# Optimization experiments

Measured on AMD Instinct MI355X. Metric: run time of the kernel, lower is better.

## Reference

```python
import jax, jax.numpy as jnp
import numpy as np

P = 8          # patch_size
DIM = 256      # embed dim
HEADS = 8
HEAD_DIM = DIM // HEADS
CH = 3
PATCH_DIM = CH * P * P  # 192
INNER = int(4.0 * DIM)  # 1024
SCALE = HEAD_DIM ** -0.5


def sine_pos_embedding(n, c, dtype=jnp.float32):
    # standard 1D sinusoidal position encoding, shape (n, c)
    pos = jnp.arange(n, dtype=jnp.float32)[:, None]            # (n,1)
    div = jnp.exp(jnp.arange(0, c, 2, dtype=jnp.float32) * (-np.log(10000.0) / c))
    pe = jnp.zeros((n, c), dtype=jnp.float32)
    pe = pe.at[:, 0::2].set(jnp.sin(pos * div))
    pe = pe.at[:, 1::2].set(jnp.cos(pos * div))
    return pe.astype(dtype)


def patchify(x):
    # (B,C,H,W) -> (B, n, p1*p2*C), matching 'b c (h p1) (w p2) -> b (h w) (p1 p2 c)'
    B, C, H, W = x.shape
    hp, wp = H // P, W // P
    x = x.reshape(B, C, hp, P, wp, P)
    x = x.transpose(0, 2, 4, 3, 5, 1)        # (B, hp, wp, p1, p2, C)
    return x.reshape(B, hp * wp, P * P * C)


def unpatchify(x, hp, wp):
    # (B, n, p1*p2*C) -> (B, C, H, W)
    B = x.shape[0]
    x = x.reshape(B, hp, wp, P, P, CH)
    x = x.transpose(0, 5, 1, 3, 2, 4)        # (B, C, hp, p1, wp, p2)
    return x.reshape(B, CH, hp * P, wp * P)


def setup_inputs() -> dict:
    key = jax.random.key(0)
    ks = jax.random.split(key, 16)
    B, H, W = 8, 256, 256
    s = 0.02
    img0 = jax.random.normal(ks[0], (B, CH, H, W), dtype=jnp.float32)
    img1 = jax.random.normal(ks[1], (B, CH, H, W), dtype=jnp.float32)
    mask = jax.random.randint(ks[2], (B, 1, H, W), 0, 2).astype(jnp.float32)
    return {
        "img0": img0,
        "img1": img1,
        "mask": mask,
        "w_patch": jax.random.normal(ks[3], (PATCH_DIM, DIM), jnp.float32) * s,
        "b_patch": jnp.zeros((DIM,), jnp.float32),
        "w_kv": jax.random.normal(ks[4], (DIM, 2 * DIM), jnp.float32) * s,
        "b_kv": jnp.zeros((2 * DIM,), jnp.float32),
        "w_qv": jax.random.normal(ks[5], (DIM, 2 * DIM), jnp.float32) * s,
        "b_qv": jnp.zeros((2 * DIM,), jnp.float32),
        "w_fc1": jax.random.normal(ks[6], (DIM, INNER), jnp.float32) * s,
        "b_fc1": jnp.zeros((INNER,), jnp.float32),
        "w_fc2": jax.random.normal(ks[7], (INNER, PATCH_DIM), jnp.float32) * s,
        "b_fc2": jnp.zeros((PATCH_DIM,), jnp.float32),
    }


def reference(img0, img1, mask, w_patch, b_patch, w_kv, b_kv, w_qv, b_qv,
              w_fc1, b_fc1, w_fc2, b_fc2):
    B, C, H, W = img0.shape
    hp, wp = H // P, W // P
    n = hp * wp

    x0 = patchify(img0) @ w_patch + b_patch   # (B, n, dim)
    x1 = patchify(img1) @ w_patch + b_patch
    pe = sine_pos_embedding(n, DIM)
    x0 = x0 + pe
    x1 = x1 + pe

    # img0 -> k, v
    kv = (x0 @ w_kv + b_kv).reshape(B, n, 2, HEADS, HEAD_DIM)
    kv = kv.transpose(2, 0, 3, 1, 4)          # (2, B, heads, n, hd)
    k, v = kv[0], kv[1]

    # img1 -> q (v1 unused in forward, matching torch code)
    qv = (x1 @ w_qv + b_qv).reshape(B, n, 2, DIM).transpose(2, 0, 1, 3)
    q = qv[0].reshape(B, n, HEADS, HEAD_DIM).transpose(0, 2, 1, 3)  # (B, heads, n, hd)

    dots = jnp.einsum('bhqd,bhkd->bhqk', q, k) * SCALE  # (B, heads, n, n)

    # mask: (B,1,H,W) -> per-patch sum -> binary -> additive bias over key dim
    msum = mask.reshape(B, 1, hp, P, wp, P).sum(axis=(3, 5)).reshape(B, 1, n)
    bias = jnp.where(msum > 0, 0.0, -100.0)[:, :, None, :]  # (B,1,1,n)

    attn = jax.nn.softmax(dots + bias, axis=-1)
    out = jnp.einsum('bhqk,bhkd->bhqd', attn, v)
    out = out.transpose(0, 2, 1, 3).reshape(B, n, DIM)

    # mlp2: Linear -> GELU(exact) -> Linear
    h = jax.nn.gelu(out @ w_fc1 + b_fc1, approximate=False)
    res = h @ w_fc2 + b_fc2                   # (B, n, patch_dim)

    return unpatchify(res, hp, wp)            # (B, C, H, W)
```

## Files before the change

### kernel.cpp

```cpp
#include <hip/hip_runtime.h>
#include <cstdint>
#include <cstddef>

typedef __bf16 bf16_t;
typedef uint32_t u32;
typedef __bf16 bf16x4 __attribute__((ext_vector_type(4)));
typedef __bf16 bf16x8 __attribute__((ext_vector_type(8)));
typedef float f32x4 __attribute__((ext_vector_type(4)));
typedef float f32x16 __attribute__((ext_vector_type(16)));

__device__ __forceinline__ void gload_lds16(const bf16_t* g, bf16_t* l) {
  __builtin_amdgcn_global_load_lds((const __attribute__((address_space(1))) void*)g,
                                   (__attribute__((address_space(3))) void*)l,
                                   16, 0, 0);
}

__device__ __forceinline__ f32x4 mfma16(bf16x8 a, bf16x8 b, f32x4 c) {
  return __builtin_amdgcn_mfma_f32_16x16x32_bf16(a, b, c, 0, 0, 0);
}
__device__ __forceinline__ f32x16 mfma32(bf16x8 a, bf16x8 b, f32x16 c) {
  return __builtin_amdgcn_mfma_f32_32x32x16_bf16(a, b, c, 0, 0, 0);
}

#define LOG2E 1.4426950408889634f

__global__ __launch_bounds__(256)
void prep_all(const float* __restrict__ img0, const float* __restrict__ img1,
              const float* __restrict__ mask,
              const float* __restrict__ wp, const float* __restrict__ wkv,
              const float* __restrict__ wqv, const float* __restrict__ wfc1,
              const float* __restrict__ wfc2,
              bf16_t* __restrict__ xp0, bf16_t* __restrict__ xp1,
              float* __restrict__ pe, float* __restrict__ bias,
              bf16_t* __restrict__ wpT, bf16_t* __restrict__ wkvT,
              bf16_t* __restrict__ wqT, bf16_t* __restrict__ wfc1T,
              bf16_t* __restrict__ wfc2T) {
  __shared__ float tl[64 * 65];
  int bid = blockIdx.x, tid = threadIdx.x;
  if (bid < 1536) {
    int imgsel = bid >= 768;
    int t = (bid - (imgsel ? 768 : 0)) * 256 + tid;
    const float* img = imgsel ? img1 : img0;
    bf16_t* xp = imgsel ? xp1 : xp0;
    int wpp = t & 31, p1 = (t >> 5) & 7, hp = (t >> 8) & 31, rest = t >> 13;
    int b = rest / 3, c = rest - b * 3;
    const float* src = img + (((size_t)(b * 3 + c) * 256 + hp * 8 + p1) * 256 + wpp * 8);
    float4 v0 = *(const float4*)src;
    float4 v1 = *(const float4*)(src + 4);
    int row = b * 1024 + hp * 32 + wpp;
    bf16_t* dst = xp + (size_t)row * 192 + p1 * 24 + c;
    dst[0]  = (bf16_t)v0.x; dst[3]  = (bf16_t)v0.y; dst[6]  = (bf16_t)v0.z; dst[9]  = (bf16_t)v0.w;
    dst[12] = (bf16_t)v1.x; dst[15] = (bf16_t)v1.y; dst[18] = (bf16_t)v1.z; dst[21] = (bf16_t)v1.w;
  } else if (bid < 2560) {
    int t = bid - 1536, c = tid;
    int i2 = c & ~1;
    float div = expf((float)i2 * (-9.210340371976184f / 256.0f));
    float arg = (float)t * div;
    pe[t * 256 + c] = (c & 1) ? cosf(arg) : sinf(arg);
  } else if (bid < 2592) {
    int g = (bid - 2560) * 256 + tid;
    int b = g >> 10, t = g & 1023, hp = t >> 5, wpp = t & 31;
    const float* mp = mask + ((size_t)b * 256 + hp * 8) * 256 + wpp * 8;
    float s = 0.f;
    #pragma unroll
    for (int p1 = 0; p1 < 8; p1++) {
      float4 a = *(const float4*)(mp + p1 * 256);
      float4 c = *(const float4*)(mp + p1 * 256 + 4);
      s += a.x + a.y + a.z + a.w + c.x + c.y + c.z + c.w;
    }
    bias[g] = (s > 0.f) ? 0.f : (-100.f * LOG2E);
  } else {
    int i = bid - 2592;
    const float* src; bf16_t* dst; int srcN, dstK, NT;
    if (i >= 172) {
      int j = i - 172;
      bf16_t* p = wfc2T + 192 * 1024 + j * 8192 + tid * 32;
      bf16x8 z;
      #pragma unroll
      for (int e = 0; e < 8; e++) z[e] = (bf16_t)0.0f;
      *(bf16x8*)(p) = z; *(bf16x8*)(p + 8) = z;
      *(bf16x8*)(p + 16) = z; *(bf16x8*)(p + 24) = z;
      return;
    }
    if (i < 12)       { src = wp;   dst = wpT;   srcN = 256;  dstK = 192;  NT = 4; }
    else if (i < 44)  { i -= 12;  src = wkv;  dst = wkvT;  srcN = 512;  dstK = 256;  NT = 8; }
    else if (i < 60)  { i -= 44;  src = wqv;  dst = wqT;   srcN = 512;  dstK = 256;  NT = 4; }
    else if (i < 124) { i -= 60;  src = wfc1; dst = wfc1T; srcN = 1024; dstK = 256;  NT = 16; }
    else              { i -= 124; src = wfc2; dst = wfc2T; srcN = 192;  dstK = 1024; NT = 3; }
    int kt = i / NT, nt = i - kt * NT;
    #pragma unroll
    for (int j = 0; j < 4; j++) {
      int r = (tid >> 4) + 16 * j, c = (tid & 15) * 4;
      float4 v = *(const float4*)(src + (size_t)(kt * 64 + r) * srcN + nt * 64 + c);
      tl[r * 65 + c] = v.x; tl[r * 65 + c + 1] = v.y;
      tl[r * 65 + c + 2] = v.z; tl[r * 65 + c + 3] = v.w;
    }
    __syncthreads();
    #pragma unroll
    for (int j = 0; j < 16; j++) {
      int flat = tid + 256 * j;
      int n_l = flat >> 6, k_l = flat & 63;
      dst[(size_t)(nt * 64 + n_l) * dstK + kt * 64 + k_l] = (bf16_t)tl[k_l * 65 + n_l];
    }
  }
}

template<int EPI, int BN>
__global__ __launch_bounds__(256)
void gemm_bt(const bf16_t* __restrict__ A_, const bf16_t* __restrict__ A2,
             const bf16_t* __restrict__ Bt_, const bf16_t* __restrict__ Bt2,
             int M, int N, int K,
             const float* __restrict__ bias_, const float* __restrict__ bias2,
             const float* __restrict__ pe,
             bf16_t* __restrict__ out_b, bf16_t* __restrict__ out_b2,
             bf16_t* __restrict__ out_b3, float* __restrict__ out_f) {
  constexpr int NF = BN / 32;
  __shared__ bf16_t alds[4 * 64 * 8];
  __shared__ bf16_t blds[4 * BN * 8];
  const int tid = threadIdx.x;
  const int lane = tid & 63, wid = tid >> 6;
  const int ln15 = lane & 15, hi = lane >> 4;
  const int brow = blockIdx.x * 64;
  int bcol = blockIdx.y * BN;
  const bf16_t* A = A_;
  const bf16_t* Bt = Bt_;
  const float* bias = bias_;
  bool qpart = false;
  if (EPI == 0 && blockIdx.z) A = A2;
  if (EPI == 5 && blockIdx.y >= 4) {
    qpart = true; A = A2; Bt = Bt2; bias = bias2; bcol -= 512;
  }
  const int wr = wid >> 1, wc = wid & 1;

  f32x4 acc[2][NF];
  #pragma unroll
  for (int m = 0; m < 2; m++)
    #pragma unroll
    for (int n = 0; n < NF; n++) acc[m][n] = (f32x4){0.f, 0.f, 0.f, 0.f};

  for (int k0 = 0; k0 < K; k0 += 32) {
    {
      int c = tid; int row = c & 63; int kb = c >> 6;
      const bf16_t* g = A + (size_t)(brow + row) * K + k0 + kb * 8;
      gload_lds16(g, &alds[(wid * 64) * 8]);
    }
    #pragma unroll
    for (int s = 0; s < BN / 64; s++) {
      int c = tid + s * 256; int row = c & (BN - 1); int kb = c / BN;
      const bf16_t* g = Bt + (size_t)(bcol + row) * K + k0 + kb * 8;
      gload_lds16(g, &blds[(wid * 64 + s * 256) * 8]);
    }
    __syncthreads();
    bf16x8 af[2], bfr[NF];
    #pragma unroll
    for (int m = 0; m < 2; m++)
      af[m] = *(const bf16x8*)&alds[(hi * 64 + wr * 32 + m * 16 + ln15) * 8];
    #pragma unroll
    for (int n = 0; n < NF; n++)
      bfr[n] = *(const bf16x8*)&blds[(hi * BN + wc * (BN / 2) + n * 16 + ln15) * 8];
    #pragma unroll
    for (int m = 0; m < 2; m++)
      #pragma unroll
      for (int n = 0; n < NF; n++)
        acc[m][n] = mfma16(af[m], bfr[n], acc[m][n]);
    __syncthreads();
  }

  #pragma unroll
  for (int m = 0; m < 2; m++) {
    #pragma unroll
    for (int n = 0; n < NF; n++) {
      #pragma unroll
      for (int r = 0; r < 4; r++) {
        int grow = brow + wr * 32 + m * 16 + hi * 4 + r;
        int gcol = bcol + wc * (BN / 2) + n * 16 + ln15;
        float v = acc[m][n][r];
        if (EPI == 0) {
          v += bias[gcol] + pe[(grow & 1023) * 256 + gcol];
          bf16_t* outx = blockIdx.z ? out_b2 : out_b;
          outx[(size_t)grow * N + gcol] = (bf16_t)v;
        } else if (EPI == 5) {
          v += bias[gcol];
          int b = grow >> 10, t = grow & 1023;
          if (!qpart) {
            if (gcol < 256) {
              int h = gcol >> 5, d = gcol & 31;
              out_b[(((size_t)(b * 8 + h) * 1024 + t) << 5) + d] = (bf16_t)v;
            } else {
              int c2 = gcol - 256; int h = c2 >> 5, d = c2 & 31;
              out_b2[(((size_t)(b * 8 + h) * 32 + d) << 10) + t] = (bf16_t)v;
            }
          } else {
            v *= (0.17677669529663687f * LOG2E);
            int h = gcol >> 5, d = gcol & 31;
            out_b3[(((size_t)(b * 8 + h) * 1024 + t) << 5) + d] = (bf16_t)v;
          }
        } else if (EPI == 3) {
          v += bias[gcol];
          float gg = 0.5f * v * (1.0f + erff(v * 0.7071067811865476f));
          out_b[(size_t)grow * N + gcol] = (bf16_t)gg;
        } else if (EPI == 4) {
          if (gcol < 192) {
            v += bias[gcol];
            int b = grow >> 10, t = grow & 1023;
            int hp = t >> 5, wpp = t & 31;
            int p = gcol / 3; int c = gcol - p * 3;
            int p1 = p >> 3, p2 = p & 7;
            out_f[(((size_t)(b * 3 + c) * 256 + hp * 8 + p1) * 256) + wpp * 8 + p2] = v;
          }
        }
      }
    }
  }
}

struct Ld { bf16x8 kA, kB, vA, vB; f32x4 c0, c1, c2, c3; };

__device__ __forceinline__ void ldstep(int k0, const bf16_t* kb, const bf16_t* vb,
                                       const float* bb, int l31, int g, Ld& L) {
  L.kA = *(const bf16x8*)(kb + (size_t)(k0 + l31) * 32 + g * 8);
  L.kB = *(const bf16x8*)(kb + (size_t)(k0 + l31) * 32 + 16 + g * 8);
  L.vA = *(const bf16x8*)(vb + (size_t)l31 * 1024 + k0 + g * 8);
  L.vB = *(const bf16x8*)(vb + (size_t)l31 * 1024 + k0 + 16 + g * 8);
  L.c0 = *(const f32x4*)(bb + k0 + 4 * g);
  L.c1 = *(const f32x4*)(bb + k0 + 8 + 4 * g);
  L.c2 = *(const f32x4*)(bb + k0 + 16 + 4 * g);
  L.c3 = *(const f32x4*)(bb + k0 + 24 + 4 * g);
}

union PW { u32 w[4]; bf16x8 v; };

__device__ __forceinline__ u32 pkbf(float a, float b) {
  union { bf16_t h[2]; u32 w; } u;
  u.h[0] = (bf16_t)a; u.h[1] = (bf16_t)b;
  return u.w;
}

__device__ __forceinline__ void step(const Ld& L, bf16x8 qf0, bf16x8 qf1, int g,
                                     f32x16& acc, f32x16& lacc, bf16x8 onesb) {
  f32x16 S;
  S[0] = L.c0[0]; S[1] = L.c0[1]; S[2] = L.c0[2]; S[3] = L.c0[3];
  S[4] = L.c1[0]; S[5] = L.c1[1]; S[6] = L.c1[2]; S[7] = L.c1[3];
  S[8] = L.c2[0]; S[9] = L.c2[1]; S[10] = L.c2[2]; S[11] = L.c2[3];
  S[12] = L.c3[0]; S[13] = L.c3[1]; S[14] = L.c3[2]; S[15] = L.c3[3];
  S = mfma32(L.kA, qf0, S);
  S = mfma32(L.kB, qf1, S);
  float p[16];
  #pragma unroll
  for (int r = 0; r < 16; r++) p[r] = exp2f(S[r]);
  u32 w[8];
  #pragma unroll
  for (int j = 0; j < 8; j++) w[j] = pkbf(p[2 * j], p[2 * j + 1]);
  u32 t0 = (u32)__shfl_xor((int)(g ? w[0] : w[2]), 32);
  u32 t1 = (u32)__shfl_xor((int)(g ? w[1] : w[3]), 32);
  u32 t2 = (u32)__shfl_xor((int)(g ? w[4] : w[6]), 32);
  u32 t3 = (u32)__shfl_xor((int)(g ? w[5] : w[7]), 32);
  PW A0, A1;
  A0.w[0] = g ? t0 : w[0];  A0.w[1] = g ? t1 : w[1];
  A0.w[2] = g ? w[2] : t0;  A0.w[3] = g ? w[3] : t1;
  A1.w[0] = g ? t2 : w[4];  A1.w[1] = g ? t3 : w[5];
  A1.w[2] = g ? w[6] : t2;  A1.w[3] = g ? w[7] : t3;
  acc = mfma32(A0.v, L.vA, acc);
  acc = mfma32(A1.v, L.vB, acc);
  lacc = mfma32(A0.v, onesb, lacc);
  lacc = mfma32(A1.v, onesb, lacc);
}

__global__ __launch_bounds__(256)
void attn_kernel(const bf16_t* __restrict__ q, const bf16_t* __restrict__ k,
                 const bf16_t* __restrict__ vt, const float* __restrict__ bias,
                 bf16_t* __restrict__ out) {
  int tid = threadIdx.x, lane = tid & 63, wid = tid >> 6;
  int l31 = lane & 31, g = lane >> 5;
  int x = blockIdx.x & 7, idx = blockIdx.x >> 3;
  int qb = idx & 7;
  int bh = ((idx >> 3) << 3) | x;
  int b = bh >> 3, h = bh & 7;
  int q0 = qb * 128 + wid * 32;
  const bf16_t* qp = q + ((size_t)bh * 1024 + q0 + l31) * 32;
  bf16x8 qf0 = *(const bf16x8*)(qp + g * 8);
  bf16x8 qf1 = *(const bf16x8*)(qp + 16 + g * 8);
  const bf16_t* kbase = k + (size_t)bh * 32768;
  const bf16_t* vbase = vt + (size_t)bh * 32768;
  const float* bb = bias + b * 1024;

  bf16x8 onesb;
  #pragma unroll
  for (int e = 0; e < 8; e++) onesb[e] = (bf16_t)1.0f;
  f32x16 acc, lacc;
  #pragma unroll
  for (int r = 0; r < 16; r++) { acc[r] = 0.f; lacc[r] = 0.f; }

  Ld La, Lb;
  ldstep(0, kbase, vbase, bb, l31, g, La);
  for (int kt = 0; kt < 32; kt += 2) {
    ldstep((kt + 1) * 32, kbase, vbase, bb, l31, g, Lb);
    step(La, qf0, qf1, g, acc, lacc, onesb);
    int nx = (kt + 2 < 32) ? (kt + 2) * 32 : 31 * 32;
    ldstep(nx, kbase, vbase, bb, l31, g, La);
    step(Lb, qf0, qf1, g, acc, lacc, onesb);
  }

  #pragma unroll
  for (int r = 0; r < 16; r++) {
    int row = (r & 3) + 8 * (r >> 2) + 4 * g;
    float o = acc[r] / lacc[r];
    out[((size_t)b * 1024 + q0 + row) * 256 + h * 32 + l31] = (bf16_t)o;
  }
}

extern "C" void kernel_launch(void* const* d_in, const int* in_sizes, int n_in,
                              void* d_out, int out_size, void* d_ws, size_t ws_size,
                              hipStream_t stream) {
  (void)in_sizes; (void)n_in; (void)out_size; (void)ws_size;
  const float* img0    = (const float*)d_in[0];
  const float* img1    = (const float*)d_in[1];
  const float* mask    = (const float*)d_in[2];
  const float* w_patch = (const float*)d_in[3];
  const float* b_patch = (const float*)d_in[4];
  const float* w_kv    = (const float*)d_in[5];
  const float* b_kv    = (const float*)d_in[6];
  const float* w_qv    = (const float*)d_in[7];
  const float* b_qv    = (const float*)d_in[8];
  const float* w_fc1   = (const float*)d_in[9];
  const float* b_fc1   = (const float*)d_in[10];
  const float* w_fc2   = (const float*)d_in[11];
  const float* b_fc2   = (const float*)d_in[12];
  float* out = (float*)d_out;

  char* ws = (char*)d_ws;
  float*  pe    = (float*)(ws + 0);
  float*  bias  = (float*)(ws + 1048576);
  bf16_t* wpT   = (bf16_t*)(ws + 1081344);
  bf16_t* wkvT  = (bf16_t*)(ws + 1179648);
  bf16_t* wqT   = (bf16_t*)(ws + 1441792);
  bf16_t* wfc1T = (bf16_t*)(ws + 1572864);
  bf16_t* wfc2T = (bf16_t*)(ws + 2097152);
  bf16_t* xp0   = (bf16_t*)(ws + 2621440);
  bf16_t* xp1   = (bf16_t*)(ws + 5767168);
  bf16_t* x0    = (bf16_t*)(ws + 8912896);
  bf16_t* x1    = (bf16_t*)(ws + 13107200);
  bf16_t* kbuf  = (bf16_t*)(ws + 17301504);
  bf16_t* vtbuf = (bf16_t*)(ws + 21495808);
  bf16_t* qbuf  = (bf16_t*)(ws + 25690112);
  bf16_t* aout  = (bf16_t*)(ws + 29884416);
  bf16_t* hbuf  = (bf16_t*)(ws + 34078720);

  prep_all<<<2772, 256, 0, stream>>>(img0, img1, mask, w_patch, w_kv, w_qv, w_fc1, w_fc2,
                                     xp0, xp1, pe, bias, wpT, wkvT, wqT, wfc1T, wfc2T);

  gemm_bt<0, 64><<<dim3(128, 4, 2), 256, 0, stream>>>(xp0, xp1, wpT, nullptr, 8192, 256, 192,
                                                      b_patch, nullptr, pe, x0, x1, nullptr, nullptr);
  gemm_bt<5, 128><<<dim3(128, 6), 256, 0, stream>>>(x0, x1, wkvT, wqT, 8192, 512, 256,
                                                    b_kv, b_qv, nullptr, kbuf, vtbuf, qbuf, nullptr);

  attn_kernel<<<512, 256, 0, stream>>>(qbuf, kbuf, vtbuf, bias, aout);

  gemm_bt<3, 128><<<dim3(128, 8), 256, 0, stream>>>(aout, nullptr, wfc1T, nullptr, 8192, 1024, 256,
                                                    b_fc1, nullptr, nullptr, hbuf, nullptr, nullptr, nullptr);
  gemm_bt<4, 64><<<dim3(128, 4), 256, 0, stream>>>(hbuf, nullptr, wfc2T, nullptr, 8192, 256, 1024,
                                                   b_fc2, nullptr, nullptr, nullptr, nullptr, nullptr, out);
}
```

Measured before the change: 126.2 us.

## Split attention keys across waves with LDS reduction and permlane swap

Restructures the attention kernel so each block handles a 32-query tile and its four waves each process a quarter of the keys, merging partial outputs and row sums through shared memory. The grid grows fourfold to raise parallelism and shorten each wave's serial loop. Row sums are now computed with scalar adds instead of an extra MFMA against a ones vector, and the cross-half shuffle is replaced with v_permlane32_swap. The cost is an LDS reduction plus a barrier per block, and the explicit double-buffered prefetch is dropped in favour of a fully unrolled loop.

```diff
diff --git a/kernel.cpp b/kernel.cpp
--- a/kernel.cpp
+++ b/kernel.cpp
@@ -214,20 +214,6 @@
   }
 }
 
-struct Ld { bf16x8 kA, kB, vA, vB; f32x4 c0, c1, c2, c3; };
-
-__device__ __forceinline__ void ldstep(int k0, const bf16_t* kb, const bf16_t* vb,
-                                       const float* bb, int l31, int g, Ld& L) {
-  L.kA = *(const bf16x8*)(kb + (size_t)(k0 + l31) * 32 + g * 8);
-  L.kB = *(const bf16x8*)(kb + (size_t)(k0 + l31) * 32 + 16 + g * 8);
-  L.vA = *(const bf16x8*)(vb + (size_t)l31 * 1024 + k0 + g * 8);
-  L.vB = *(const bf16x8*)(vb + (size_t)l31 * 1024 + k0 + 16 + g * 8);
-  L.c0 = *(const f32x4*)(bb + k0 + 4 * g);
-  L.c1 = *(const f32x4*)(bb + k0 + 8 + 4 * g);
-  L.c2 = *(const f32x4*)(bb + k0 + 16 + 4 * g);
-  L.c3 = *(const f32x4*)(bb + k0 + 24 + 4 * g);
-}
-
 union PW { u32 w[4]; bf16x8 v; };
 
 __device__ __forceinline__ u32 pkbf(float a, float b) {
@@ -236,47 +222,23 @@
   return u.w;
 }
 
-__device__ __forceinline__ void step(const Ld& L, bf16x8 qf0, bf16x8 qf1, int g,
-                                     f32x16& acc, f32x16& lacc, bf16x8 onesb) {
-  f32x16 S;
-  S[0] = L.c0[0]; S[1] = L.c0[1]; S[2] = L.c0[2]; S[3] = L.c0[3];
-  S[4] = L.c1[0]; S[5] = L.c1[1]; S[6] = L.c1[2]; S[7] = L.c1[3];
-  S[8] = L.c2[0]; S[9] = L.c2[1]; S[10] = L.c2[2]; S[11] = L.c2[3];
-  S[12] = L.c3[0]; S[13] = L.c3[1]; S[14] = L.c3[2]; S[15] = L.c3[3];
-  S = mfma32(L.kA, qf0, S);
-  S = mfma32(L.kB, qf1, S);
-  float p[16];
-  #pragma unroll
-  for (int r = 0; r < 16; r++) p[r] = exp2f(S[r]);
-  u32 w[8];
-  #pragma unroll
-  for (int j = 0; j < 8; j++) w[j] = pkbf(p[2 * j], p[2 * j + 1]);
-  u32 t0 = (u32)__shfl_xor((int)(g ? w[0] : w[2]), 32);
-  u32 t1 = (u32)__shfl_xor((int)(g ? w[1] : w[3]), 32);
-  u32 t2 = (u32)__shfl_xor((int)(g ? w[4] : w[6]), 32);
-  u32 t3 = (u32)__shfl_xor((int)(g ? w[5] : w[7]), 32);
-  PW A0, A1;
-  A0.w[0] = g ? t0 : w[0];  A0.w[1] = g ? t1 : w[1];
-  A0.w[2] = g ? w[2] : t0;  A0.w[3] = g ? w[3] : t1;
-  A1.w[0] = g ? t2 : w[4];  A1.w[1] = g ? t3 : w[5];
-  A1.w[2] = g ? w[6] : t2;  A1.w[3] = g ? w[7] : t3;
-  acc = mfma32(A0.v, L.vA, acc);
-  acc = mfma32(A1.v, L.vB, acc);
-  lacc = mfma32(A0.v, onesb, lacc);
-  lacc = mfma32(A1.v, onesb, lacc);
-}
-
-__global__ __launch_bounds__(256)
+__device__ __forceinline__ void pl32swap(u32& a, u32& b) {
+  asm volatile("v_permlane32_swap_b32 %0, %1" : "+v"(a), "+v"(b));
+}
+
+__global__ __launch_bounds__(256, 4)
 void attn_kernel(const bf16_t* __restrict__ q, const bf16_t* __restrict__ k,
                  const bf16_t* __restrict__ vt, const float* __restrict__ bias,
                  bf16_t* __restrict__ out) {
+  __shared__ float OL[4][32][34];
+  __shared__ float LS[4][64];
   int tid = threadIdx.x, lane = tid & 63, wid = tid >> 6;
   int l31 = lane & 31, g = lane >> 5;
-  int x = blockIdx.x & 7, idx = blockIdx.x >> 3;
-  int qb = idx & 7;
-  int bh = ((idx >> 3) << 3) | x;
+  int x = blockIdx.x & 7;
+  int bh = (((blockIdx.x >> 3) & 7) << 3) | x;
+  int qt = blockIdx.x >> 6;
   int b = bh >> 3, h = bh & 7;
-  int q0 = qb * 128 + wid * 32;
+  int q0 = qt * 32;
   const bf16_t* qp = q + ((size_t)bh * 1024 + q0 + l31) * 32;
   bf16x8 qf0 = *(const bf16x8*)(qp + g * 8);
   bf16x8 qf1 = *(const bf16x8*)(qp + 16 + g * 8);
@@ -284,29 +246,73 @@
   const bf16_t* vbase = vt + (size_t)bh * 32768;
   const float* bb = bias + b * 1024;
 
-  bf16x8 onesb;
-  #pragma unroll
-  for (int e = 0; e < 8; e++) onesb[e] = (bf16_t)1.0f;
-  f32x16 acc, lacc;
-  #pragma unroll
-  for (int r = 0; r < 16; r++) { acc[r] = 0.f; lacc[r] = 0.f; }
-
-  Ld La, Lb;
-  ldstep(0, kbase, vbase, bb, l31, g, La);
-  for (int kt = 0; kt < 32; kt += 2) {
-    ldstep((kt + 1) * 32, kbase, vbase, bb, l31, g, Lb);
-    step(La, qf0, qf1, g, acc, lacc, onesb);
-    int nx = (kt + 2 < 32) ? (kt + 2) * 32 : 31 * 32;
-    ldstep(nx, kbase, vbase, bb, l31, g, La);
-    step(Lb, qf0, qf1, g, acc, lacc, onesb);
+  f32x16 acc;
+  #pragma unroll
+  for (int r = 0; r < 16; r++) acc[r] = 0.f;
+  float lsum = 0.f;
+
+  #pragma unroll
+  for (int kt = 0; kt < 8; kt++) {
+    int k0 = (wid * 8 + kt) * 32;
+    bf16x8 kA = *(const bf16x8*)(kbase + (size_t)(k0 + l31) * 32 + g * 8);
+    bf16x8 kB = *(const bf16x8*)(kbase + (size_t)(k0 + l31) * 32 + 16 + g * 8);
+    bf16x8 vA = *(const bf16x8*)(vbase + (size_t)l31 * 1024 + k0 + g * 8);
+    bf16x8 vB = *(const bf16x8*)(vbase + (size_t)l31 * 1024 + k0 + 16 + g * 8);
+    f32x4 c0 = *(const f32x4*)(bb + k0 + 4 * g);
+    f32x4 c1 = *(const f32x4*)(bb + k0 + 8 + 4 * g);
+    f32x4 c2 = *(const f32x4*)(bb + k0 + 16 + 4 * g);
+    f32x4 c3 = *(const f32x4*)(bb + k0 + 24 + 4 * g);
+    f32x16 S;
+    S[0] = c0[0]; S[1] = c0[1]; S[2] = c0[2]; S[3] = c0[3];
+    S[4] = c1[0]; S[5] = c1[1]; S[6] = c1[2]; S[7] = c1[3];
+    S[8] = c2[0]; S[9] = c2[1]; S[10] = c2[2]; S[11] = c2[3];
+    S[12] = c3[0]; S[13] = c3[1]; S[14] = c3[2]; S[15] = c3[3];
+    S = mfma32(kA, qf0, S);
+    S = mfma32(kB, qf1, S);
+    float p[16];
+    #pragma unroll
+    for (int r = 0; r < 16; r++) p[r] = exp2f(S[r]);
+    lsum += (((p[0] + p[1]) + (p[2] + p[3])) + ((p[4] + p[5]) + (p[6] + p[7]))) +
+            (((p[8] + p[9]) + (p[10] + p[11])) + ((p[12] + p[13]) + (p[14] + p[15])));
+    u32 w[8];
+    #pragma unroll
+    for (int j = 0; j < 8; j++) w[j] = pkbf(p[2 * j], p[2 * j + 1]);
+    u32 xa = w[2], ya = w[0]; pl32swap(xa, ya);
+    u32 xb = w[3], yb = w[1]; pl32swap(xb, yb);
+    u32 xc = w[6], yc = w[4]; pl32swap(xc, yc);
+    u32 xd = w[7], yd = w[5]; pl32swap(xd, yd);
+    PW A0, A1;
+    A0.w[0] = g ? xa : w[0];  A0.w[2] = g ? w[2] : ya;
+    A0.w[1] = g ? xb : w[1];  A0.w[3] = g ? w[3] : yb;
+    A1.w[0] = g ? xc : w[4];  A1.w[2] = g ? w[6] : yc;
+    A1.w[1] = g ? xd : w[5];  A1.w[3] = g ? w[7] : yd;
+    acc = mfma32(A0.v, vA, acc);
+    acc = mfma32(A1.v, vB, acc);
   }
 
   #pragma unroll
   for (int r = 0; r < 16; r++) {
     int row = (r & 3) + 8 * (r >> 2) + 4 * g;
-    float o = acc[r] / lacc[r];
-    out[((size_t)b * 1024 + q0 + row) * 256 + h * 32 + l31] = (bf16_t)o;
-  }
+    OL[wid][row][l31] = acc[r];
+  }
+  LS[wid][lane] = lsum;
+  __syncthreads();
+
+  int qq = tid >> 3, d0 = (tid & 7) * 4;
+  float l = 0.f;
+  #pragma unroll
+  for (int w2 = 0; w2 < 4; w2++) l += LS[w2][qq] + LS[w2][32 + qq];
+  float o0 = 0.f, o1 = 0.f, o2 = 0.f, o3 = 0.f;
+  #pragma unroll
+  for (int w2 = 0; w2 < 4; w2++) {
+    o0 += OL[w2][qq][d0];     o1 += OL[w2][qq][d0 + 1];
+    o2 += OL[w2][qq][d0 + 2]; o3 += OL[w2][qq][d0 + 3];
+  }
+  float linv = 1.f / l;
+  bf16x4 ov;
+  ov[0] = (bf16_t)(o0 * linv); ov[1] = (bf16_t)(o1 * linv);
+  ov[2] = (bf16_t)(o2 * linv); ov[3] = (bf16_t)(o3 * linv);
+  *(bf16x4*)(out + ((size_t)b * 1024 + q0 + qq) * 256 + h * 32 + d0) = ov;
 }
 
 extern "C" void kernel_launch(void* const* d_in, const int* in_sizes, int n_in,
@@ -354,7 +360,7 @@
   gemm_bt<5, 128><<<dim3(128, 6), 256, 0, stream>>>(x0, x1, wkvT, wqT, 8192, 512, 256,
                                                     b_kv, b_qv, nullptr, kbuf, vtbuf, qbuf, nullptr);
 
-  attn_kernel<<<512, 256, 0, stream>>>(qbuf, kbuf, vtbuf, bias, aout);
+  attn_kernel<<<2048, 256, 0, stream>>>(qbuf, kbuf, vtbuf, bias, aout);
 
   gemm_bt<3, 128><<<dim3(128, 8), 256, 0, stream>>>(aout, nullptr, wfc1T, nullptr, 8192, 1024, 256,
                                                     b_fc1, nullptr, nullptr, hbuf, nullptr, nullptr, nullptr);
```

Measured after the change: 122.9 us. 1.03x faster.
